# Optimization experiments

Hardware: AMD Instinct MI355X
Metric: run time of the kernel (lower is better)

Reference implementation:

```python
import jax, jax.numpy as jnp
import numpy as np

EPS = 1e-12  # F.normalize default eps

def setup_inputs() -> dict:
    key = jax.random.key(0)
    k1, k2, k3 = jax.random.split(key, 3)
    content = jax.random.normal(k1, (64, 512, 32, 32), dtype=jnp.float32)
    bank_content = jax.random.normal(k2, (256, 524288), dtype=jnp.float32)
    bank_style = jax.random.normal(k3, (256, 2048), dtype=jnp.float32)
    return {"content": content, "bank_content": bank_content, "bank_style": bank_style}

def reference(content, bank_content, bank_style):
    B = content.shape[0]
    M = bank_content.shape[0]
    # L2-normalize flattened queries along feature dim
    cs = content.reshape(B, -1)                                   # [B, D]
    cs = cs / jnp.maximum(jnp.linalg.norm(cs, axis=1, keepdims=True), EPS)
    # NOTE: original uses view(-1, M) -> raw row-major reshape, not a transpose
    ct = bank_content.reshape(-1, M)                              # [D, M]
    ct = ct / jnp.maximum(jnp.linalg.norm(ct, axis=0, keepdims=True), EPS)
    sim = cs @ ct                                                 # [B, M]
    idx = jnp.argmax(sim, axis=1)                                 # [B]
    return bank_style[idx]                                        # [B, S]
```

## Files before the change

kernel.cpp:

```cpp
#include <hip/hip_runtime.h>

#define BQ 64
#define MB 256
#define DK 524288
#define SS 2048
#define CH 32
#define TPB 256

__global__ __launch_bounds__(TPB, 4) void k1_partial(
    const float* __restrict__ content, const float* __restrict__ bank,
    float* __restrict__ psim, float* __restrict__ pcn, int G)
{
    __shared__ float cs_t[CH * BQ];
    __shared__ float ct_t[CH * MB];
    const int tid = threadIdx.x;
    const int g   = blockIdx.x;
    const int tb  = tid & 7;
    const int tm  = tid >> 3;

    float acc[8][8];
    #pragma unroll
    for (int i = 0; i < 8; ++i)
        #pragma unroll
        for (int j = 0; j < 8; ++j) acc[i][j] = 0.f;
    float cn0 = 0.f, cn1 = 0.f, cn2 = 0.f, cn3 = 0.f;

    const int NC = DK / CH;
    for (int c = g; c < NC; c += G) {
        const int d0 = c * CH;
        __syncthreads();
        {
            const float4* src = (const float4*)(bank + (size_t)d0 * MB);
            float4* dst = (float4*)ct_t;
            #pragma unroll
            for (int k = 0; k < 8; ++k) {
                float4 v = src[tid + k * 256];
                dst[tid + k * 256] = v;
                cn0 = fmaf(v.x, v.x, cn0);
                cn1 = fmaf(v.y, v.y, cn1);
                cn2 = fmaf(v.z, v.z, cn2);
                cn3 = fmaf(v.w, v.w, cn3);
            }
        }
        #pragma unroll
        for (int p = 0; p < 2; ++p) {
            int q  = tid + p * 256;
            int b  = q >> 3, c4 = q & 7;
            float4 v = *(const float4*)(content + (size_t)b * DK + d0 + c4 * 4);
            int dd = c4 * 4;
            cs_t[(dd + 0) * BQ + b] = v.x;
            cs_t[(dd + 1) * BQ + b] = v.y;
            cs_t[(dd + 2) * BQ + b] = v.z;
            cs_t[(dd + 3) * BQ + b] = v.w;
        }
        __syncthreads();
        #pragma unroll 2
        for (int d = 0; d < CH; ++d) {
            float4 a0 = *(const float4*)&cs_t[d * BQ + tb * 8];
            float4 a1 = *(const float4*)&cs_t[d * BQ + tb * 8 + 4];
            float4 b0 = *(const float4*)&ct_t[d * MB + tm * 8];
            float4 b1 = *(const float4*)&ct_t[d * MB + tm * 8 + 4];
            float av[8] = {a0.x, a0.y, a0.z, a0.w, a1.x, a1.y, a1.z, a1.w};
            float bv[8] = {b0.x, b0.y, b0.z, b0.w, b1.x, b1.y, b1.z, b1.w};
            #pragma unroll
            for (int i = 0; i < 8; ++i)
                #pragma unroll
                for (int j = 0; j < 8; ++j)
                    acc[i][j] = fmaf(av[i], bv[j], acc[i][j]);
        }
    }

    {
        float* outp = psim + (size_t)g * (BQ * MB);
        #pragma unroll
        for (int i = 0; i < 8; ++i) {
            int b = tb * 8 + i;
            *(float4*)&outp[b * MB + tm * 8] =
                make_float4(acc[i][0], acc[i][1], acc[i][2], acc[i][3]);
            *(float4*)&outp[b * MB + tm * 8 + 4] =
                make_float4(acc[i][4], acc[i][5], acc[i][6], acc[i][7]);
        }
    }
    __syncthreads();
    *(float4*)&ct_t[tid * 4] = make_float4(cn0, cn1, cn2, cn3);
    __syncthreads();
    {
        int m = tid;
        int tsrc = m >> 2, comp = m & 3;
        float v = ct_t[(tsrc      ) * 4 + comp]
                + ct_t[(tsrc +  64) * 4 + comp]
                + ct_t[(tsrc + 128) * 4 + comp]
                + ct_t[(tsrc + 192) * 4 + comp];
        pcn[(size_t)g * MB + m] = v;
    }
}

__global__ void k2_reduce(const float* __restrict__ psim,
                          const float* __restrict__ pcn,
                          float* __restrict__ stage2, int G)
{
    const int r  = blockIdx.x % 65;
    const int gs = blockIdx.x / 65;
    const int o  = r * 256 + threadIdx.x;
    float s = 0.f;
    if (o < BQ * MB) {
        for (int g = gs; g < G; g += 8) s += psim[(size_t)g * (BQ * MB) + o];
    } else {
        int m = o - BQ * MB;
        for (int g = gs; g < G; g += 8) s += pcn[(size_t)g * MB + m];
    }
    stage2[(size_t)gs * 16640 + o] = s;
}

__global__ void k3_argmax_gather(const float* __restrict__ stage2,
                                 const float* __restrict__ bank_style,
                                 float* __restrict__ out)
{
    const int b = blockIdx.x;
    const int tid = threadIdx.x;
    float s = 0.f, c = 0.f;
    #pragma unroll
    for (int gs = 0; gs < 8; ++gs) {
        s += stage2[(size_t)gs * 16640 + b * MB + tid];
        c += stage2[(size_t)gs * 16640 + BQ * MB + tid];
    }
    float score = s / fmaxf(sqrtf(c), 1e-12f);

    float best = score; int bidx = tid;
    #pragma unroll
    for (int off = 32; off >= 1; off >>= 1) {
        float os = __shfl_down(best, off);
        int   oi = __shfl_down(bidx, off);
        if (os > best || (os == best && oi < bidx)) { best = os; bidx = oi; }
    }
    __shared__ float wbest[4];
    __shared__ int   widx[4];
    __shared__ int   fidx;
    int wave = tid >> 6, lane = tid & 63;
    if (lane == 0) { wbest[wave] = best; widx[wave] = bidx; }
    __syncthreads();
    if (tid == 0) {
        float fb = wbest[0]; int fi = widx[0];
        #pragma unroll
        for (int w = 1; w < 4; ++w)
            if (wbest[w] > fb || (wbest[w] == fb && widx[w] < fi)) {
                fb = wbest[w]; fi = widx[w];
            }
        fidx = fi;
    }
    __syncthreads();
    const float4* srcr = (const float4*)(bank_style + (size_t)fidx * SS);
    float4*       dstr = (float4*)(out + (size_t)b * SS);
    for (int k = tid; k < SS / 4; k += TPB) dstr[k] = srcr[k];
}

extern "C" void kernel_launch(void* const* d_in, const int* in_sizes, int n_in,
                              void* d_out, int out_size, void* d_ws, size_t ws_size,
                              hipStream_t stream)
{
    const float* content      = (const float*)d_in[0];
    const float* bank_content = (const float*)d_in[1];
    const float* bank_style   = (const float*)d_in[2];
    float* out = (float*)d_out;

    long long avail = (long long)(ws_size / 4) - 8LL * 16640;
    int G = (int)(avail / 16640);
    if (G > 1024) G = 1024;
    if (G < 1)    G = 1;

    float* psim   = (float*)d_ws;
    float* pcn    = psim + (size_t)G * (BQ * MB);
    float* stage2 = psim + (size_t)G * 16640;

    k1_partial<<<G, TPB, 0, stream>>>(content, bank_content, psim, pcn, G);
    k2_reduce<<<520, TPB, 0, stream>>>(psim, pcn, stage2, G);
    k3_argmax_gather<<<BQ, TPB, 0, stream>>>(stage2, bank_style, out);
}
```

Baseline: 863.8 us.

## Double-buffer shared tiles with register prefetch of next chunk in k1_partial

Splits the depth chunk from 32 to 16 and adds two shared-memory buffers for both the bank and content tiles. Global loads for the next chunk go into registers before the FMA loop on the current buffer and are stored to the other buffer afterwards, so load latency overlaps compute and one barrier per iteration is enough. The cost is more registers for the prefetched values and twice as many loop iterations, with more barrier and store overhead relative to compute.

Result: no change. 852.4 us (-1.3%).

```diff
diff --git a/kernel.cpp b/kernel.cpp
--- a/kernel.cpp
+++ b/kernel.cpp
@@ -4,15 +4,16 @@
 #define MB 256
 #define DK 524288
 #define SS 2048
-#define CH 32
+#define CH 16
 #define TPB 256
+#define NCHUNK (DK / CH)
 
 __global__ __launch_bounds__(TPB, 4) void k1_partial(
     const float* __restrict__ content, const float* __restrict__ bank,
     float* __restrict__ psim, float* __restrict__ pcn, int G)
 {
-    __shared__ float cs_t[CH * BQ];
-    __shared__ float ct_t[CH * MB];
+    __shared__ float ct_t[2][CH * MB];
+    __shared__ float cs_t[2][CH * BQ];
     const int tid = threadIdx.x;
     const int g   = blockIdx.x;
     const int tb  = tid & 7;
@@ -25,41 +26,58 @@
         for (int j = 0; j < 8; ++j) acc[i][j] = 0.f;
     float cn0 = 0.f, cn1 = 0.f, cn2 = 0.f, cn3 = 0.f;
 
-    const int NC = DK / CH;
-    for (int c = g; c < NC; c += G) {
-        const int d0 = c * CH;
-        __syncthreads();
-        {
-            const float4* src = (const float4*)(bank + (size_t)d0 * MB);
-            float4* dst = (float4*)ct_t;
-            #pragma unroll
-            for (int k = 0; k < 8; ++k) {
-                float4 v = src[tid + k * 256];
-                dst[tid + k * 256] = v;
-                cn0 = fmaf(v.x, v.x, cn0);
-                cn1 = fmaf(v.y, v.y, cn1);
-                cn2 = fmaf(v.z, v.z, cn2);
-                cn3 = fmaf(v.w, v.w, cn3);
-            }
-        }
-        #pragma unroll
-        for (int p = 0; p < 2; ++p) {
-            int q  = tid + p * 256;
-            int b  = q >> 3, c4 = q & 7;
-            float4 v = *(const float4*)(content + (size_t)b * DK + d0 + c4 * 4);
-            int dd = c4 * 4;
-            cs_t[(dd + 0) * BQ + b] = v.x;
-            cs_t[(dd + 1) * BQ + b] = v.y;
-            cs_t[(dd + 2) * BQ + b] = v.z;
-            cs_t[(dd + 3) * BQ + b] = v.w;
-        }
-        __syncthreads();
+    const float4* bank4 = (const float4*)bank;
+    const int csb_b  = tid >> 2;
+    const int csb_c4 = tid & 3;
+    const float* cs_src = content + (size_t)csb_b * DK + csb_c4 * 4;
+
+    float4 rct0, rct1, rct2, rct3;
+    float4 rcs;
+
+    {
+        const size_t base = (size_t)g * 1024 + tid;
+        rct0 = bank4[base];           rct1 = bank4[base + 256];
+        rct2 = bank4[base + 512];     rct3 = bank4[base + 768];
+        rcs  = *(const float4*)(cs_src + (size_t)g * CH);
+    }
+    {
+        float4* dst = (float4*)ct_t[0];
+        dst[tid]       = rct0;  dst[tid + 256] = rct1;
+        dst[tid + 512] = rct2;  dst[tid + 768] = rct3;
+        cn0 = fmaf(rct0.x, rct0.x, cn0); cn1 = fmaf(rct0.y, rct0.y, cn1);
+        cn2 = fmaf(rct0.z, rct0.z, cn2); cn3 = fmaf(rct0.w, rct0.w, cn3);
+        cn0 = fmaf(rct1.x, rct1.x, cn0); cn1 = fmaf(rct1.y, rct1.y, cn1);
+        cn2 = fmaf(rct1.z, rct1.z, cn2); cn3 = fmaf(rct1.w, rct1.w, cn3);
+        cn0 = fmaf(rct2.x, rct2.x, cn0); cn1 = fmaf(rct2.y, rct2.y, cn1);
+        cn2 = fmaf(rct2.z, rct2.z, cn2); cn3 = fmaf(rct2.w, rct2.w, cn3);
+        cn0 = fmaf(rct3.x, rct3.x, cn0); cn1 = fmaf(rct3.y, rct3.y, cn1);
+        cn2 = fmaf(rct3.z, rct3.z, cn2); cn3 = fmaf(rct3.w, rct3.w, cn3);
+        const int dd = csb_c4 * 4;
+        cs_t[0][(dd + 0) * BQ + csb_b] = rcs.x;
+        cs_t[0][(dd + 1) * BQ + csb_b] = rcs.y;
+        cs_t[0][(dd + 2) * BQ + csb_b] = rcs.z;
+        cs_t[0][(dd + 3) * BQ + csb_b] = rcs.w;
+    }
+    __syncthreads();
+
+    int cur = 0;
+    for (int c = g; c < NCHUNK; c += G) {
+        const int nxt = c + G;
+        const bool have = (nxt < NCHUNK);
+        if (have) {
+            const size_t base = (size_t)nxt * 1024 + tid;
+            rct0 = bank4[base];           rct1 = bank4[base + 256];
+            rct2 = bank4[base + 512];     rct3 = bank4[base + 768];
+            rcs  = *(const float4*)(cs_src + (size_t)nxt * CH);
+        }
+        const float* csb = cs_t[cur];
+        const float* ctb = ct_t[cur];
         #pragma unroll 2
         for (int d = 0; d < CH; ++d) {
-            float4 a0 = *(const float4*)&cs_t[d * BQ + tb * 8];
-            float4 a1 = *(const float4*)&cs_t[d * BQ + tb * 8 + 4];
-            float4 b0 = *(const float4*)&ct_t[d * MB + tm * 8];
-            float4 b1 = *(const float4*)&ct_t[d * MB + tm * 8 + 4];
+            float4 a0 = *(const float4*)&csb[d * BQ + tb * 8];
+            float4 a1 = *(const float4*)&csb[d * BQ + tb * 8 + 4];
+            float4 b0 = *(const float4*)&ctb[d * MB + tm * 8];
+            float4 b1 = *(const float4*)&ctb[d * MB + tm * 8 + 4];
             float av[8] = {a0.x, a0.y, a0.z, a0.w, a1.x, a1.y, a1.z, a1.w};
             float bv[8] = {b0.x, b0.y, b0.z, b0.w, b1.x, b1.y, b1.z, b1.w};
             #pragma unroll
@@ -68,6 +86,27 @@
                 for (int j = 0; j < 8; ++j)
                     acc[i][j] = fmaf(av[i], bv[j], acc[i][j]);
         }
+        if (have) {
+            float4* dst = (float4*)ct_t[cur ^ 1];
+            dst[tid]       = rct0;  dst[tid + 256] = rct1;
+            dst[tid + 512] = rct2;  dst[tid + 768] = rct3;
+            cn0 = fmaf(rct0.x, rct0.x, cn0); cn1 = fmaf(rct0.y, rct0.y, cn1);
+            cn2 = fmaf(rct0.z, rct0.z, cn2); cn3 = fmaf(rct0.w, rct0.w, cn3);
+            cn0 = fmaf(rct1.x, rct1.x, cn0); cn1 = fmaf(rct1.y, rct1.y, cn1);
+            cn2 = fmaf(rct1.z, rct1.z, cn2); cn3 = fmaf(rct1.w, rct1.w, cn3);
+            cn0 = fmaf(rct2.x, rct2.x, cn0); cn1 = fmaf(rct2.y, rct2.y, cn1);
+            cn2 = fmaf(rct2.z, rct2.z, cn2); cn3 = fmaf(rct2.w, rct2.w, cn3);
+            cn0 = fmaf(rct3.x, rct3.x, cn0); cn1 = fmaf(rct3.y, rct3.y, cn1);
+            cn2 = fmaf(rct3.z, rct3.z, cn2); cn3 = fmaf(rct3.w, rct3.w, cn3);
+            const int dd = csb_c4 * 4;
+            float* dcs = cs_t[cur ^ 1];
+            dcs[(dd + 0) * BQ + csb_b] = rcs.x;
+            dcs[(dd + 1) * BQ + csb_b] = rcs.y;
+            dcs[(dd + 2) * BQ + csb_b] = rcs.z;
+            dcs[(dd + 3) * BQ + csb_b] = rcs.w;
+        }
+        __syncthreads();
+        cur ^= 1;
     }
 
     {
@@ -82,15 +121,15 @@
         }
     }
     __syncthreads();
-    *(float4*)&ct_t[tid * 4] = make_float4(cn0, cn1, cn2, cn3);
+    *(float4*)&ct_t[0][tid * 4] = make_float4(cn0, cn1, cn2, cn3);
     __syncthreads();
     {
         int m = tid;
         int tsrc = m >> 2, comp = m & 3;
-        float v = ct_t[(tsrc      ) * 4 + comp]
-                + ct_t[(tsrc +  64) * 4 + comp]
-                + ct_t[(tsrc + 128) * 4 + comp]
-                + ct_t[(tsrc + 192) * 4 + comp];
+        float v = ct_t[0][(tsrc      ) * 4 + comp]
+                + ct_t[0][(tsrc +  64) * 4 + comp]
+                + ct_t[0][(tsrc + 128) * 4 + comp]
+                + ct_t[0][(tsrc + 192) * 4 + comp];
         pcn[(size_t)g * MB + m] = v;
     }
 }
```

## Use split-bf16 MFMA for similarity GEMM with register-prefetched chunk pipeline

Applied to the files above, without the earlier changes.

Replaces the FP32 FMA outer-product inner loop with bf16 MFMA 16x16x32 instructions. Each fp32 operand is split into a high and a low bf16 part, and three products are accumulated to keep the result close to fp32 accuracy. Global loads for the next chunk are prefetched into registers while the current chunk is computed. Occupancy hints and grid size are changed as well. The aim is to move the matmul onto the matrix cores, with some loss of precision that could flip argmax ties, plus extra conversion work.

After: 821.6 us. 1.05x faster.

```diff
diff --git a/kernel.cpp b/kernel.cpp
--- a/kernel.cpp
+++ b/kernel.cpp
@@ -6,91 +6,157 @@
 #define SS 2048
 #define CH 32
 #define TPB 256
-
-__global__ __launch_bounds__(TPB, 4) void k1_partial(
+#define NCHUNK (DK / CH)
+
+#define SA 40
+#define SB 260
+
+typedef __attribute__((ext_vector_type(8))) short short8;
+typedef __attribute__((ext_vector_type(4))) float f32x4;
+
+__device__ __forceinline__ unsigned short bf16_rne(float x) {
+    unsigned int u = __float_as_uint(x);
+    return (unsigned short)((u + 0x7FFFu + ((u >> 16) & 1u)) >> 16);
+}
+__device__ __forceinline__ float bf16_f32(unsigned short h) {
+    return __uint_as_float((unsigned int)h << 16);
+}
+
+__global__ __launch_bounds__(TPB, 2) void k1_partial(
     const float* __restrict__ content, const float* __restrict__ bank,
     float* __restrict__ psim, float* __restrict__ pcn, int G)
 {
-    __shared__ float cs_t[CH * BQ];
-    __shared__ float ct_t[CH * MB];
-    const int tid = threadIdx.x;
-    const int g   = blockIdx.x;
-    const int tb  = tid & 7;
-    const int tm  = tid >> 3;
-
-    float acc[8][8];
+    __shared__ unsigned short A_hi[BQ * SA];
+    __shared__ unsigned short A_lo[BQ * SA];
+    __shared__ unsigned short B_hi[CH * SB];
+    __shared__ unsigned short B_lo[CH * SB];
+    __shared__ float cnscr[TPB * 4];
+
+    const int tid  = threadIdx.x;
+    const int g    = blockIdx.x;
+    const int w    = tid >> 6;
+    const int l    = tid & 63;
+    const int rowl = l & 15;
+    const int kg   = l >> 4;
+
+    f32x4 acc[4][4];
     #pragma unroll
-    for (int i = 0; i < 8; ++i)
-        #pragma unroll
-        for (int j = 0; j < 8; ++j) acc[i][j] = 0.f;
+    for (int i = 0; i < 4; ++i)
+        #pragma unroll
+        for (int j = 0; j < 4; ++j) acc[i][j] = (f32x4){0.f, 0.f, 0.f, 0.f};
+
     float cn0 = 0.f, cn1 = 0.f, cn2 = 0.f, cn3 = 0.f;
 
-    const int NC = DK / CH;
-    for (int c = g; c < NC; c += G) {
-        const int d0 = c * CH;
+    const float4* bank4 = (const float4*)bank;
+    float4 rb[8];
+    float4 rc[2];
+
+    auto load_chunk = [&](int c) {
+        const float4* bsrc = bank4 + (size_t)c * (CH * MB / 4);
+        #pragma unroll
+        for (int q = 0; q < 8; ++q) rb[q] = bsrc[tid + (q << 8)];
+        #pragma unroll
+        for (int q = 0; q < 2; ++q) {
+            const int b = (w << 3) + (q << 5) + (l >> 3);
+            rc[q] = *(const float4*)(content + (size_t)b * DK
+                                     + (size_t)c * CH + ((l & 7) << 2));
+        }
+    };
+    auto store_chunk = [&]() {
+        #pragma unroll
+        for (int q = 0; q < 8; ++q) {
+            const int d = w + (q << 2);
+            const float4 v = rb[q];
+            const unsigned short h0 = bf16_rne(v.x), h1 = bf16_rne(v.y),
+                                 h2 = bf16_rne(v.z), h3 = bf16_rne(v.w);
+            const unsigned short e0 = bf16_rne(v.x - bf16_f32(h0)),
+                                 e1 = bf16_rne(v.y - bf16_f32(h1)),
+                                 e2 = bf16_rne(v.z - bf16_f32(h2)),
+                                 e3 = bf16_rne(v.w - bf16_f32(h3));
+            *(short4*)&B_hi[d * SB + (l << 2)] =
+                make_short4((short)h0, (short)h1, (short)h2, (short)h3);
+            *(short4*)&B_lo[d * SB + (l << 2)] =
+                make_short4((short)e0, (short)e1, (short)e2, (short)e3);
+            cn0 = fmaf(v.x, v.x, cn0);  cn1 = fmaf(v.y, v.y, cn1);
+            cn2 = fmaf(v.z, v.z, cn2);  cn3 = fmaf(v.w, v.w, cn3);
+        }
+        #pragma unroll
+        for (int q = 0; q < 2; ++q) {
+            const int b = (w << 3) + (q << 5) + (l >> 3);
+            const float4 v = rc[q];
+            const unsigned short h0 = bf16_rne(v.x), h1 = bf16_rne(v.y),
+                                 h2 = bf16_rne(v.z), h3 = bf16_rne(v.w);
+            const unsigned short e0 = bf16_rne(v.x - bf16_f32(h0)),
+                                 e1 = bf16_rne(v.y - bf16_f32(h1)),
+                                 e2 = bf16_rne(v.z - bf16_f32(h2)),
+                                 e3 = bf16_rne(v.w - bf16_f32(h3));
+            *(short4*)&A_hi[b * SA + ((l & 7) << 2)] =
+                make_short4((short)h0, (short)h1, (short)h2, (short)h3);
+            *(short4*)&A_lo[b * SA + ((l & 7) << 2)] =
+                make_short4((short)e0, (short)e1, (short)e2, (short)e3);
+        }
+    };
+
+    load_chunk(g);
+    store_chunk();
+    __syncthreads();
+
+    for (int c = g; c < NCHUNK; c += G) {
+        const int nxt = c + G;
+        const bool have = (nxt < NCHUNK);
+        if (have) load_chunk(nxt);
+
+        #pragma unroll
+        for (int mt = 0; mt < 4; ++mt) {
+            const int colo = (w << 6) + (mt << 4) + rowl;
+            short8 bhv, blv;
+            #pragma unroll
+            for (int j = 0; j < 8; ++j) {
+                const int ro = ((kg << 3) + j) * SB + colo;
+                bhv[j] = (short)B_hi[ro];
+                blv[j] = (short)B_lo[ro];
+            }
+            #pragma unroll
+            for (int bt = 0; bt < 4; ++bt) {
+                const int ao = ((bt << 4) + rowl) * SA + (kg << 3);
+                const short8 ahv = *(const short8*)&A_hi[ao];
+                const short8 alv = *(const short8*)&A_lo[ao];
+                acc[bt][mt] = __builtin_amdgcn_mfma_f32_16x16x32_bf16(
+                                  ahv, bhv, acc[bt][mt], 0, 0, 0);
+                acc[bt][mt] = __builtin_amdgcn_mfma_f32_16x16x32_bf16(
+                                  alv, bhv, acc[bt][mt], 0, 0, 0);
+                acc[bt][mt] = __builtin_amdgcn_mfma_f32_16x16x32_bf16(
+                                  ahv, blv, acc[bt][mt], 0, 0, 0);
+            }
+        }
         __syncthreads();
-        {
-            const float4* src = (const float4*)(bank + (size_t)d0 * MB);
-            float4* dst = (float4*)ct_t;
-            #pragma unroll
-            for (int k = 0; k < 8; ++k) {
-                float4 v = src[tid + k * 256];
-                dst[tid + k * 256] = v;
-                cn0 = fmaf(v.x, v.x, cn0);
-                cn1 = fmaf(v.y, v.y, cn1);
-                cn2 = fmaf(v.z, v.z, cn2);
-                cn3 = fmaf(v.w, v.w, cn3);
-            }
-        }
-        #pragma unroll
-        for (int p = 0; p < 2; ++p) {
-            int q  = tid + p * 256;
-            int b  = q >> 3, c4 = q & 7;
-            float4 v = *(const float4*)(content + (size_t)b * DK + d0 + c4 * 4);
-            int dd = c4 * 4;
-            cs_t[(dd + 0) * BQ + b] = v.x;
-            cs_t[(dd + 1) * BQ + b] = v.y;
-            cs_t[(dd + 2) * BQ + b] = v.z;
-            cs_t[(dd + 3) * BQ + b] = v.w;
-        }
+        if (have) store_chunk();
         __syncthreads();
-        #pragma unroll 2
-        for (int d = 0; d < CH; ++d) {
-            float4 a0 = *(const float4*)&cs_t[d * BQ + tb * 8];
-            float4 a1 = *(const float4*)&cs_t[d * BQ + tb * 8 + 4];
-            float4 b0 = *(const float4*)&ct_t[d * MB + tm * 8];
-            float4 b1 = *(const float4*)&ct_t[d * MB + tm * 8 + 4];
-            float av[8] = {a0.x, a0.y, a0.z, a0.w, a1.x, a1.y, a1.z, a1.w};
-            float bv[8] = {b0.x, b0.y, b0.z, b0.w, b1.x, b1.y, b1.z, b1.w};
-            #pragma unroll
-            for (int i = 0; i < 8; ++i)
-                #pragma unroll
-                for (int j = 0; j < 8; ++j)
-                    acc[i][j] = fmaf(av[i], bv[j], acc[i][j]);
-        }
     }
 
     {
         float* outp = psim + (size_t)g * (BQ * MB);
         #pragma unroll
-        for (int i = 0; i < 8; ++i) {
-            int b = tb * 8 + i;
-            *(float4*)&outp[b * MB + tm * 8] =
-                make_float4(acc[i][0], acc[i][1], acc[i][2], acc[i][3]);
-            *(float4*)&outp[b * MB + tm * 8 + 4] =
-                make_float4(acc[i][4], acc[i][5], acc[i][6], acc[i][7]);
-        }
-    }
-    __syncthreads();
-    *(float4*)&ct_t[tid * 4] = make_float4(cn0, cn1, cn2, cn3);
+        for (int bt = 0; bt < 4; ++bt)
+            #pragma unroll
+            for (int mt = 0; mt < 4; ++mt) {
+                const int m = (w << 6) + (mt << 4) + rowl;
+                #pragma unroll
+                for (int i = 0; i < 4; ++i) {
+                    const int b = (bt << 4) + (kg << 2) + i;
+                    outp[b * MB + m] = acc[bt][mt][i];
+                }
+            }
+    }
+    *(float4*)&cnscr[tid * 4] = make_float4(cn0, cn1, cn2, cn3);
     __syncthreads();
     {
-        int m = tid;
-        int tsrc = m >> 2, comp = m & 3;
-        float v = ct_t[(tsrc      ) * 4 + comp]
-                + ct_t[(tsrc +  64) * 4 + comp]
-                + ct_t[(tsrc + 128) * 4 + comp]
-                + ct_t[(tsrc + 192) * 4 + comp];
+        const int m = tid;
+        const int tsrc = m >> 2, comp = m & 3;
+        float v = cnscr[(tsrc      ) * 4 + comp]
+                + cnscr[(tsrc +  64) * 4 + comp]
+                + cnscr[(tsrc + 128) * 4 + comp]
+                + cnscr[(tsrc + 192) * 4 + comp];
         pcn[(size_t)g * MB + m] = v;
     }
 }
@@ -165,8 +231,8 @@
 
     long long avail = (long long)(ws_size / 4) - 8LL * 16640;
     int G = (int)(avail / 16640);
-    if (G > 1024) G = 1024;
-    if (G < 1)    G = 1;
+    if (G > 768) G = 768;
+    if (G < 1)   G = 1;
 
     float* psim   = (float*)d_ws;
     float* pcn    = psim + (size_t)G * (BQ * MB);
```
